# Performance work log

Measured on AMD Instinct MI355X. Metric: run time of the kernel, lower is better.

The kernel has to match this reference:

```python
import jax, jax.numpy as jnp
import numpy as np

H, W, R = 512, 512, 4
H8, W8 = H // 8, W // 8  # 64, 64
B, C = 4, 256


def _offsets(r):
    # diamond window: y in [-r, r], x in [|y|-r, r-|y|]  ->  2r^2+2r+1 offsets
    offs = []
    for y in range(-r, r + 1):
        for x in range(abs(y) - r, r - abs(y) + 1):
            offs.append((y, x))
    return np.asarray(offs, dtype=np.float32)  # [L, 2] = (dy, dx)

_OFFS = _offsets(R)  # L = 41


def _corr_pyramid(f1, f2):
    # over the second image's spatial dims for each pyramid level.
    c = jnp.einsum('bcij,bcuv->bijuv', f1, f2) / jnp.sqrt(jnp.float32(f1.shape[1]))
    pyr = [c]
    for _ in range(3):
        b, i, j, h, w = pyr[-1].shape
        pyr.append(pyr[-1].reshape(b, i, j, h // 2, 2, w // 2, 2).mean(axis=(4, 6)))
    return pyr  # shapes [B,64,64,64/2^k,64/2^k] for k=0..3


def _bilinear_zeros(volf, py, px, h, w):
    # volf: [B,H8,W8,h*w]; py/px: [B,H8,W8,L] pixel coords; zero padding.
    y0 = jnp.floor(py); x0 = jnp.floor(px)
    wy1 = py - y0; wy0 = 1.0 - wy1
    wx1 = px - x0; wx0 = 1.0 - wx1

    def gather(yi, xi):
        valid = (yi >= 0) & (yi < h) & (xi >= 0) & (xi < w)
        yc = jnp.clip(yi, 0, h - 1).astype(jnp.int32)
        xc = jnp.clip(xi, 0, w - 1).astype(jnp.int32)
        v = jnp.take_along_axis(volf, yc * w + xc, axis=-1)
        return jnp.where(valid, v, jnp.zeros((), volf.dtype))

    return (wy0 * wx0 * gather(y0, x0) + wy0 * wx1 * gather(y0, x0 + 1)
            + wy1 * wx0 * gather(y0 + 1, x0) + wy1 * wx1 * gather(y0 + 1, x0 + 1))


def _lookup_level(corr, flow, k):
    # corr: [B,H8,W8,h,w]; flow: [B,2,H8,W8] (chan 0 = dy, chan 1 = dx)
    b, _, _, h, w = corr.shape
    dy = jnp.asarray(_OFFS[:, 0]); dx = jnp.asarray(_OFFS[:, 1])
    ii = jnp.arange(H8, dtype=corr.dtype)[:, None]   # [H8,1]
    jj = jnp.arange(W8, dtype=corr.dtype)[None, :]   # [1,W8]
    scale = jnp.float32(2.0 ** k)
    yc = (ii[None] + flow[:, 0]) / scale             # [B,H8,W8]
    xc = (jj[None] + flow[:, 1]) / scale
    py = yc[..., None] + dy                          # [B,H8,W8,L]
    px = xc[..., None] + dx
    # original normalizes by dim/2 (not (dim-1)/2), grid_sample align_corners=True
    # maps normalized g -> pixel (g+1)*(dim-1)/2, net: pixel = coord*(dim-1)/dim
    py = py * (h - 1) / h
    px = px * (w - 1) / w
    volf = corr.reshape(b, H8, W8, h * w)
    return _bilinear_zeros(volf, py, px, h, w)       # [B,H8,W8,L]


def setup_inputs() -> dict:
    key = jax.random.key(0)
    k1, k2, k3 = jax.random.split(key, 3)
    feat1 = jax.random.normal(k1, (B, C, H8, W8), dtype=jnp.float32)
    feat2 = jax.random.normal(k2, (B, C, H8, W8), dtype=jnp.float32)
    curr_flow = jax.random.normal(k3, (B, 2, H8, W8), dtype=jnp.float32)
    return {"feat1": feat1, "feat2": feat2, "curr_flow": curr_flow}


def reference(feat1, feat2, curr_flow):
    pyr = _corr_pyramid(feat1, feat2)
    lookups = [_lookup_level(pyr[k], curr_flow, k) for k in range(4)]
    return jnp.stack(lookups, axis=3)  # [B, H8, W8, 4, 41]
```

## Files before the change

kernel.cpp:

```cpp
#include <hip/hip_runtime.h>
#include <stdint.h>

#define NB 4
#define NC 256
#define TC 5440

typedef short bf16x8 __attribute__((ext_vector_type(8)));
typedef float f32x4  __attribute__((ext_vector_type(4)));

__device__ __forceinline__ unsigned short f2b(float x){
  uint32_t u = __float_as_uint(x);
  return (unsigned short)((u + 0x7FFFu + ((u >> 16) & 1u)) >> 16);
}

__global__ __launch_bounds__(256) void prep_all(const float* __restrict__ f1,
                 const float* __restrict__ f2,
                 unsigned short* __restrict__ f1t,
                 unsigned short* __restrict__ f2p){
  __shared__ float lds[128*65];
  const int t = threadIdx.x;
  const int bx = blockIdx.x;

  if (bx < 2048){
    const int b = bx >> 9, rest = bx & 511;
    const int cc = rest >> 7, pt = rest & 127;
    const int p0 = pt*32, c0 = cc*64;
    const int tx = t & 31, ty = t >> 5;
    float (*tileF)[33] = (float(*)[33])lds;
    #pragma unroll
    for (int r = 0; r < 8; ++r){
      int c = ty + r*8;
      tileF[c][tx] = f1[((size_t)(b*NC) + c0 + c)*4096 + p0 + tx];
    }
    __syncthreads();
    #pragma unroll
    for (int r = 0; r < 4; ++r){
      int pl = ty + r*8;
      size_t o = ((size_t)(b*4096 + p0 + pl))*NC;
      unsigned int v = (unsigned int)f2b(tileF[2*tx][pl])
                     | ((unsigned int)f2b(tileF[2*tx+1][pl]) << 16);
      *(unsigned int*)(f1t + o + c0 + 2*tx) = v;
    }
  } else {
    const int fid = bx - 2048;
    const int b = fid >> 7, rest = fid & 127;
    const int reg = rest >> 2, cc = rest & 3;
    const int i0 = (reg >> 2) * 8, j0 = (reg & 3) * 16;
    const int c0 = cc * 64;

    #pragma unroll
    for (int it = 0; it < 8; ++it){
      int q = t + 256*it;
      int ch = q >> 5, rc = q & 31, ri = rc >> 2, c4 = rc & 3;
      const float4 v = *(const float4*)(f2 + ((size_t)(b*NC) + c0 + ch)*4096
                                          + (i0+ri)*64 + j0 + c4*4);
      float* dstL = lds + (ri*16 + c4*4)*65 + ch;
      dstL[0] = v.x; dstL[65] = v.y; dstL[130] = v.z; dstL[195] = v.w;
    }
    __syncthreads();
    unsigned short* f2pB = f2p + (size_t)b*TC*NC;

    {
      const int u = t & 31, cb = t >> 5;
      #pragma unroll
      for (int it = 0; it < 16; ++it){
        int l = cb + 8*it;
        int ci = l >> 4, cj = l & 15;
        unsigned int v = (unsigned int)f2b(lds[l*65 + 2*u])
                       | ((unsigned int)f2b(lds[l*65 + 2*u + 1]) << 16);
        *(unsigned int*)(f2pB + ((size_t)((i0+ci)*64 + j0+cj))*NC + c0 + 2*u) = v;
      }
    }
    #pragma unroll
    for (int it = 0; it < 8; ++it){
      int idx = t + 256*it;
      int cl = idx >> 6, ch = idx & 63;
      int a = cl >> 3, bc = cl & 7;
      const float* p00 = lds + ((2*a)*16 + 2*bc)*65 + ch;
      float s = p00[0] + p00[65] + p00[16*65] + p00[17*65];
      f2pB[((size_t)(4096 + ((i0>>1)+a)*32 + (j0>>1)+bc))*NC + c0 + ch] = f2b(s*0.25f);
    }
    #pragma unroll
    for (int it = 0; it < 2; ++it){
      int idx = t + 256*it;
      int cl = idx >> 6, ch = idx & 63;
      int a = cl >> 2, bc = cl & 3;
      float s = 0.f;
      #pragma unroll
      for (int dy2 = 0; dy2 < 4; ++dy2)
        #pragma unroll
        for (int dx2 = 0; dx2 < 4; ++dx2)
          s += lds[((4*a+dy2)*16 + 4*bc+dx2)*65 + ch];
      f2pB[((size_t)(5120 + ((i0>>2)+a)*16 + (j0>>2)+bc))*NC + c0 + ch] = f2b(s*0.0625f);
    }
    if (t < 128){
      int cl = t >> 6, ch = t & 63;
      float s = 0.f;
      #pragma unroll
      for (int dy3 = 0; dy3 < 8; ++dy3)
        #pragma unroll
        for (int dx3 = 0; dx3 < 8; ++dx3)
          s += lds[(dy3*16 + 8*cl + dx3)*65 + ch];
      f2pB[((size_t)(5376 + (i0>>3)*8 + (j0>>3) + cl))*NC + c0 + ch] = f2b(s*(1.0f/64.0f));
    }
  }
}

__global__ __launch_bounds__(256, 4) void lookup_main(const float* __restrict__ flow,
                 const unsigned short* __restrict__ f1t,
                 const unsigned short* __restrict__ f2p,
                 float* __restrict__ out){
  const int lane = threadIdx.x & 63;
  const int wid  = threadIdx.x >> 6;
  const int blk = blockIdx.x;
  const int xs = blk & 7;
  const int bb = xs >> 1;
  const int tile = ((blk >> 3) << 1) | (xs & 1);
  const int ti4 = (tile >> 4) << 2;
  const int tj4 = (tile & 15) << 2;

  __shared__ float box[4*16*112];
  __shared__ int   ls_y0[64], ls_x0[64];
  __shared__ float ls_f[32];
  __shared__ int   ls_meta[32];

  {
    float4* b4 = (float4*)box;
    for (int q = threadIdx.x; q < (4*16*112)/4; q += 256)
      b4[q] = make_float4(0.f, 0.f, 0.f, 0.f);
  }

  const int n = lane & 15;
  const int g = lane >> 4;
  const int pn = ((ti4 + (n >> 2)) << 6) + tj4 + (n & 3);

  bf16x8 bfr[8];
  {
    const unsigned short* f1c = f1t + ((size_t)(bb*4096 + pn))*NC;
    #pragma unroll
    for (int st = 0; st < 8; ++st)
      bfr[st] = *(const bf16x8*)(f1c + st*32 + g*8);
  }

  if (wid == 0){
    const int k = g;
    const int i_n = pn >> 6, j_n = pn & 63;
    const float fy = flow[((bb*2 + 0)*64 + i_n)*64 + j_n];
    const float fx = flow[((bb*2 + 1)*64 + i_n)*64 + j_n];
    if (k == 0){ ls_f[n] = fy; ls_f[16 + n] = fx; }
    const int h = 64 >> k;
    const float inv = 1.0f / (float)(1 << k);
    const float s = (float)(h - 1) / (float)h;
    const float yc = ((float)i_n + fy) * inv;
    const float xc = ((float)j_n + fx) * inv;
    const int y0 = (int)floorf((yc - 4.0f) * s);
    const int x0 = (int)floorf((xc - 4.0f) * s);
    ls_y0[k*16 + n] = y0;
    ls_x0[k*16 + n] = x0;
    int ymin = y0, ymax = y0, xmin = x0, xmax = x0;
    #pragma unroll
    for (int m = 1; m < 16; m <<= 1){
      ymin = min(ymin, __shfl_xor(ymin, m));
      ymax = max(ymax, __shfl_xor(ymax, m));
      xmin = min(xmin, __shfl_xor(xmin, m));
      xmax = max(xmax, __shfl_xor(xmax, m));
    }
    if (n == 0){
      int ylo = max(ymin, 0), yhi = min(ymax + 9, h - 1);
      int xlo = max(xmin, 0), xhi = min(xmax + 9, h - 1);
      int H = max(yhi - ylo + 1, 0), W = max(xhi - xlo + 1, 0);
      int cells = W * H;
      ls_meta[k*8 + 0] = ylo;
      ls_meta[k*8 + 1] = xlo;
      ls_meta[k*8 + 2] = W;
      ls_meta[k*8 + 3] = cells;
      ls_meta[k*8 + 4] = __float_as_int(1.0f / (float)W);
      ls_meta[k*8 + 5] = (k==0) ? 0 : (k==1) ? 4096 : (k==2) ? 5120 : 5376;
      ls_meta[k*8 + 6] = (cells + 15) >> 4;
    }
  }
  __syncthreads();

  const int y0n0 = ls_y0[n],      x0n0 = ls_x0[n];
  const int y0n1 = ls_y0[16 + n], x0n1 = ls_x0[16 + n];
  const int y0n2 = ls_y0[32 + n], x0n2 = ls_x0[32 + n];
  const int y0n3 = ls_y0[48 + n], x0n3 = ls_x0[48 + n];
  const int pre1 = ls_meta[6];
  const int pre2 = pre1 + ls_meta[14];
  const int pre3 = pre2 + ls_meta[22];
  const int P    = pre3 + ls_meta[30];

  for (int p = wid; p < P; p += 4){
    const int k  = (p >= pre1) + (p >= pre2) + (p >= pre3);
    const int lp = p - ((k==0) ? 0 : (k==1) ? pre1 : (k==2) ? pre2 : pre3);
    const int mb = k*8;
    const int ylo = ls_meta[mb], xlo = ls_meta[mb+1], W = ls_meta[mb+2];
    const int cells = ls_meta[mb+3];
    const float rW = __int_as_float(ls_meta[mb+4]);
    const int lvo = ls_meta[mb+5];
    const int h = 64 >> k;
    const int base = lp << 4;

    const int idxA = min(base + n, cells - 1);
    const int by = (int)fmaf((float)idxA, rW, 0.004f);
    const int bx = idxA - by*W;
    const unsigned short* col = f2p + ((size_t)bb*TC + lvo + (ylo + by)*h + (xlo + bx))*NC;

    f32x4 acc0 = {0.f,0.f,0.f,0.f}, acc1 = {0.f,0.f,0.f,0.f};
    #pragma unroll
    for (int st = 0; st < 8; st += 2){
      bf16x8 a0 = *(const bf16x8*)(col + st*32 + g*8);
      bf16x8 a1 = *(const bf16x8*)(col + (st+1)*32 + g*8);
      acc0 = __builtin_amdgcn_mfma_f32_16x16x32_bf16(a0, bfr[st],   acc0, 0, 0, 0);
      acc1 = __builtin_amdgcn_mfma_f32_16x16x32_bf16(a1, bfr[st+1], acc1, 0, 0, 0);
    }
    const int yb = (k==0) ? y0n0 : (k==1) ? y0n1 : (k==2) ? y0n2 : y0n3;
    const int xb = (k==0) ? x0n0 : (k==1) ? x0n1 : (k==2) ? x0n2 : x0n3;
    #pragma unroll
    for (int r = 0; r < 4; ++r){
      const int ci = base + (g << 2) + r;
      if (ci < cells){
        const int byc = (int)fmaf((float)ci, rW, 0.004f);
        const int bxc = ci - byc*W;
        const int ry = ylo + byc - yb;
        const int rx = xlo + bxc - xb;
        if ((unsigned)ry < 10u && (unsigned)rx < 10u)
          box[(k*16 + n)*112 + ry*10 + rx] = (acc0[r] + acc1[r]) * 0.0625f;
      }
    }
  }
  __syncthreads();

  int dy = 0, dx = 0;
  {
    int rem = lane;
    #pragma unroll
    for (int ry = -4; ry <= 4; ++ry){
      int ab = ry < 0 ? -ry : ry;
      int ln = 9 - 2*ab;
      if (rem >= 0 && rem < ln){ dy = ry; dx = rem + (ab - 4); }
      rem -= ln;
    }
  }
  const int k = wid;
  const float inv = 1.0f / (float)(1 << k);
  const float s = (float)((64 >> k) - 1) / (float)(64 >> k);
  if (lane < 41){
    for (int t = 0; t < 16; ++t){
      const int pt = ((ti4 + (t >> 2)) << 6) + tj4 + (t & 3);
      const float fy = ls_f[t], fx = ls_f[16 + t];
      const float yc = ((float)(pt >> 6) + fy) * inv;
      const float xc = ((float)(pt & 63) + fx) * inv;
      const float py = (yc + (float)dy) * s;
      const float px = (xc + (float)dx) * s;
      const float fy0 = floorf(py), fx0 = floorf(px);
      const float wy1 = py - fy0, wx1 = px - fx0;
      const float wy0 = 1.0f - wy1, wx0 = 1.0f - wx1;
      const int iy = (int)fy0 - ls_y0[k*16 + t];
      const int ix = (int)fx0 - ls_x0[k*16 + t];
      const float* bx_ = &box[(k*16 + t)*112 + iy*10 + ix];
      const float v = wy0*(wx0*bx_[0] + wx1*bx_[1]) + wy1*(wx0*bx_[10] + wx1*bx_[11]);
      out[((size_t)(bb*4096 + pt)*4 + k)*41 + lane] = v;
    }
  }
}

extern "C" void kernel_launch(void* const* d_in, const int* in_sizes, int n_in,
                              void* d_out, int out_size, void* d_ws, size_t ws_size,
                              hipStream_t stream){
  const float* feat1 = (const float*)d_in[0];
  const float* feat2 = (const float*)d_in[1];
  const float* flow  = (const float*)d_in[2];
  float* out = (float*)d_out;
  unsigned short* f1t = (unsigned short*)d_ws;
  unsigned short* f2p = f1t + (size_t)NB*4096*NC;

  prep_all<<<2560, 256, 0, stream>>>(feat1, feat2, f1t, f2p);
  lookup_main<<<1024, 256, 0, stream>>>(flow, f1t, f2p, out);
}
```

Measured before the change: 125.6 us.

## Split lookup blocks per pyramid level to shrink LDS and raise parallelism

Each lookup block now handles a single pyramid level for its 16-pixel tile, and the grid grows to four times as many blocks. Every wave computes the per-level bounding box itself with shuffles, so the serial wave-0 metadata phase and its shared-memory table go away. The per-block box buffer shrinks to one level with a 113 stride to cut LDS bank conflicts, and the final interpolation spreads the 16 pixels across the four waves. In exchange, the f1 fragment and flow loads are repeated four times across blocks, and the coarse-level blocks get very little MFMA work.

```diff
diff --git a/kernel.cpp b/kernel.cpp
--- a/kernel.cpp
+++ b/kernel.cpp
@@ -115,18 +115,19 @@
   const int blk = blockIdx.x;
   const int xs = blk & 7;
   const int bb = xs >> 1;
-  const int tile = ((blk >> 3) << 1) | (xs & 1);
+  const int r8 = blk >> 3;
+  const int k  = r8 & 3;
+  const int tile = ((r8 >> 2) << 1) | (xs & 1);
   const int ti4 = (tile >> 4) << 2;
   const int tj4 = (tile & 15) << 2;
 
-  __shared__ float box[4*16*112];
-  __shared__ int   ls_y0[64], ls_x0[64];
+  __shared__ float box[16*113 + 4];
   __shared__ float ls_f[32];
-  __shared__ int   ls_meta[32];
+  __shared__ int   ls_y0[16], ls_x0[16];
 
   {
     float4* b4 = (float4*)box;
-    for (int q = threadIdx.x; q < (4*16*112)/4; q += 256)
+    for (int q = threadIdx.x; q < (16*113 + 4)/4; q += 256)
       b4[q] = make_float4(0.f, 0.f, 0.f, 0.f);
   }
 
@@ -142,69 +143,45 @@
       bfr[st] = *(const bf16x8*)(f1c + st*32 + g*8);
   }
 
-  if (wid == 0){
-    const int k = g;
-    const int i_n = pn >> 6, j_n = pn & 63;
-    const float fy = flow[((bb*2 + 0)*64 + i_n)*64 + j_n];
-    const float fx = flow[((bb*2 + 1)*64 + i_n)*64 + j_n];
-    if (k == 0){ ls_f[n] = fy; ls_f[16 + n] = fx; }
-    const int h = 64 >> k;
-    const float inv = 1.0f / (float)(1 << k);
-    const float s = (float)(h - 1) / (float)h;
-    const float yc = ((float)i_n + fy) * inv;
-    const float xc = ((float)j_n + fx) * inv;
-    const int y0 = (int)floorf((yc - 4.0f) * s);
-    const int x0 = (int)floorf((xc - 4.0f) * s);
-    ls_y0[k*16 + n] = y0;
-    ls_x0[k*16 + n] = x0;
-    int ymin = y0, ymax = y0, xmin = x0, xmax = x0;
-    #pragma unroll
-    for (int m = 1; m < 16; m <<= 1){
-      ymin = min(ymin, __shfl_xor(ymin, m));
-      ymax = max(ymax, __shfl_xor(ymax, m));
-      xmin = min(xmin, __shfl_xor(xmin, m));
-      xmax = max(xmax, __shfl_xor(xmax, m));
-    }
-    if (n == 0){
-      int ylo = max(ymin, 0), yhi = min(ymax + 9, h - 1);
-      int xlo = max(xmin, 0), xhi = min(xmax + 9, h - 1);
-      int H = max(yhi - ylo + 1, 0), W = max(xhi - xlo + 1, 0);
-      int cells = W * H;
-      ls_meta[k*8 + 0] = ylo;
-      ls_meta[k*8 + 1] = xlo;
-      ls_meta[k*8 + 2] = W;
-      ls_meta[k*8 + 3] = cells;
-      ls_meta[k*8 + 4] = __float_as_int(1.0f / (float)W);
-      ls_meta[k*8 + 5] = (k==0) ? 0 : (k==1) ? 4096 : (k==2) ? 5120 : 5376;
-      ls_meta[k*8 + 6] = (cells + 15) >> 4;
-    }
+  const int h = 64 >> k;
+  const float inv = 1.0f / (float)(1 << k);
+  const float s = (float)(h - 1) / (float)h;
+  const int i_n = pn >> 6, j_n = pn & 63;
+  const float fy = flow[((bb*2 + 0)*64 + i_n)*64 + j_n];
+  const float fx = flow[((bb*2 + 1)*64 + i_n)*64 + j_n];
+  const float yc = ((float)i_n + fy) * inv;
+  const float xc = ((float)j_n + fx) * inv;
+  const int y0 = (int)floorf((yc - 4.0f) * s);
+  const int x0 = (int)floorf((xc - 4.0f) * s);
+  int ymin = y0, ymax = y0, xmin = x0, xmax = x0;
+  #pragma unroll
+  for (int m = 1; m < 16; m <<= 1){
+    ymin = min(ymin, __shfl_xor(ymin, m));
+    ymax = max(ymax, __shfl_xor(ymax, m));
+    xmin = min(xmin, __shfl_xor(xmin, m));
+    xmax = max(xmax, __shfl_xor(xmax, m));
+  }
+  const int ylo = max(ymin, 0), yhi = min(ymax + 9, h - 1);
+  const int xlo = max(xmin, 0), xhi = min(xmax + 9, h - 1);
+  const int W = max(xhi - xlo + 1, 0);
+  const int cells = W * max(yhi - ylo + 1, 0);
+  const float rW = 1.0f / (float)W;
+  const int lvo = (k==0) ? 0 : (k==1) ? 4096 : (k==2) ? 5120 : 5376;
+  const unsigned short* lv = f2p + ((size_t)bb*TC + lvo)*NC;
+
+  if (threadIdx.x < 16){
+    ls_f[n] = fy; ls_f[16 + n] = fx;
+    ls_y0[n] = y0; ls_x0[n] = x0;
   }
   __syncthreads();
 
-  const int y0n0 = ls_y0[n],      x0n0 = ls_x0[n];
-  const int y0n1 = ls_y0[16 + n], x0n1 = ls_x0[16 + n];
-  const int y0n2 = ls_y0[32 + n], x0n2 = ls_x0[32 + n];
-  const int y0n3 = ls_y0[48 + n], x0n3 = ls_x0[48 + n];
-  const int pre1 = ls_meta[6];
-  const int pre2 = pre1 + ls_meta[14];
-  const int pre3 = pre2 + ls_meta[22];
-  const int P    = pre3 + ls_meta[30];
-
+  const int P = (cells + 15) >> 4;
   for (int p = wid; p < P; p += 4){
-    const int k  = (p >= pre1) + (p >= pre2) + (p >= pre3);
-    const int lp = p - ((k==0) ? 0 : (k==1) ? pre1 : (k==2) ? pre2 : pre3);
-    const int mb = k*8;
-    const int ylo = ls_meta[mb], xlo = ls_meta[mb+1], W = ls_meta[mb+2];
-    const int cells = ls_meta[mb+3];
-    const float rW = __int_as_float(ls_meta[mb+4]);
-    const int lvo = ls_meta[mb+5];
-    const int h = 64 >> k;
-    const int base = lp << 4;
-
+    const int base = p << 4;
     const int idxA = min(base + n, cells - 1);
     const int by = (int)fmaf((float)idxA, rW, 0.004f);
     const int bx = idxA - by*W;
-    const unsigned short* col = f2p + ((size_t)bb*TC + lvo + (ylo + by)*h + (xlo + bx))*NC;
+    const unsigned short* col = lv + (size_t)((ylo + by)*h + (xlo + bx))*NC;
 
     f32x4 acc0 = {0.f,0.f,0.f,0.f}, acc1 = {0.f,0.f,0.f,0.f};
     #pragma unroll
@@ -214,18 +191,16 @@
       acc0 = __builtin_amdgcn_mfma_f32_16x16x32_bf16(a0, bfr[st],   acc0, 0, 0, 0);
       acc1 = __builtin_amdgcn_mfma_f32_16x16x32_bf16(a1, bfr[st+1], acc1, 0, 0, 0);
     }
-    const int yb = (k==0) ? y0n0 : (k==1) ? y0n1 : (k==2) ? y0n2 : y0n3;
-    const int xb = (k==0) ? x0n0 : (k==1) ? x0n1 : (k==2) ? x0n2 : x0n3;
     #pragma unroll
     for (int r = 0; r < 4; ++r){
       const int ci = base + (g << 2) + r;
       if (ci < cells){
         const int byc = (int)fmaf((float)ci, rW, 0.004f);
         const int bxc = ci - byc*W;
-        const int ry = ylo + byc - yb;
-        const int rx = xlo + bxc - xb;
+        const int ry = ylo + byc - y0;
+        const int rx = xlo + bxc - x0;
         if ((unsigned)ry < 10u && (unsigned)rx < 10u)
-          box[(k*16 + n)*112 + ry*10 + rx] = (acc0[r] + acc1[r]) * 0.0625f;
+          box[n*113 + ry*10 + rx] = (acc0[r] + acc1[r]) * 0.0625f;
       }
     }
   }
@@ -242,23 +217,22 @@
       rem -= ln;
     }
   }
-  const int k = wid;
-  const float inv = 1.0f / (float)(1 << k);
-  const float s = (float)((64 >> k) - 1) / (float)(64 >> k);
   if (lane < 41){
-    for (int t = 0; t < 16; ++t){
+    #pragma unroll
+    for (int tt = 0; tt < 4; ++tt){
+      const int t = wid*4 + tt;
       const int pt = ((ti4 + (t >> 2)) << 6) + tj4 + (t & 3);
-      const float fy = ls_f[t], fx = ls_f[16 + t];
-      const float yc = ((float)(pt >> 6) + fy) * inv;
-      const float xc = ((float)(pt & 63) + fx) * inv;
-      const float py = (yc + (float)dy) * s;
-      const float px = (xc + (float)dx) * s;
+      const float fyt = ls_f[t], fxt = ls_f[16 + t];
+      const float yct = ((float)(pt >> 6) + fyt) * inv;
+      const float xct = ((float)(pt & 63) + fxt) * inv;
+      const float py = (yct + (float)dy) * s;
+      const float px = (xct + (float)dx) * s;
       const float fy0 = floorf(py), fx0 = floorf(px);
       const float wy1 = py - fy0, wx1 = px - fx0;
       const float wy0 = 1.0f - wy1, wx0 = 1.0f - wx1;
-      const int iy = (int)fy0 - ls_y0[k*16 + t];
-      const int ix = (int)fx0 - ls_x0[k*16 + t];
-      const float* bx_ = &box[(k*16 + t)*112 + iy*10 + ix];
+      const int iy = (int)fy0 - ls_y0[t];
+      const int ix = (int)fx0 - ls_x0[t];
+      const float* bx_ = &box[t*113 + iy*10 + ix];
       const float v = wy0*(wx0*bx_[0] + wx1*bx_[1]) + wy1*(wx0*bx_[10] + wx1*bx_[11]);
       out[((size_t)(bb*4096 + pt)*4 + k)*41 + lane] = v;
     }
@@ -276,5 +250,5 @@
   unsigned short* f2p = f1t + (size_t)NB*4096*NC;
 
   prep_all<<<2560, 256, 0, stream>>>(feat1, feat2, f1t, f2p);
-  lookup_main<<<1024, 256, 0, stream>>>(flow, f1t, f2p, out);
-}
+  lookup_main<<<4096, 256, 0, stream>>>(flow, f1t, f2p, out);
+}
```

After: 152.7 us. 1.22x slower.

## Store f2 pyramid in channel-chunk-major layout for coalesced MFMA gathers

Applied to the files above, without the earlier changes.

The pooled f2 pyramid changes from cell-major with 256 contiguous channels to a per-level layout of 8-channel chunks, cell-major within each chunk. Neighbouring cells read by adjacent lanes in the lookup kernel then fall on contiguous 16-byte segments rather than rows 512 bytes apart, which should improve load coalescing in the gather loop. The prep kernel now builds each pyramid level from the level above through small LDS buffers and writes 16-byte vector stores. The per-point LDS box stride is padded from 112 to 113 to reduce bank conflicts. The extra LDS and barriers in prep add some cost there.

```diff
diff --git a/kernel.cpp b/kernel.cpp
--- a/kernel.cpp
+++ b/kernel.cpp
@@ -3,7 +3,10 @@
 
 #define NB 4
 #define NC 256
-#define TC 5440
+#define FB   1392640
+#define LVO1 1048576
+#define LVO2 1310720
+#define LVO3 1376256
 
 typedef short bf16x8 __attribute__((ext_vector_type(8)));
 typedef float f32x4  __attribute__((ext_vector_type(4)));
@@ -12,12 +15,17 @@
   uint32_t u = __float_as_uint(x);
   return (unsigned short)((u + 0x7FFFu + ((u >> 16) & 1u)) >> 16);
 }
+__device__ __forceinline__ unsigned int pack2(float a, float b){
+  return (unsigned int)f2b(a) | ((unsigned int)f2b(b) << 16);
+}
 
 __global__ __launch_bounds__(256) void prep_all(const float* __restrict__ f1,
                  const float* __restrict__ f2,
                  unsigned short* __restrict__ f1t,
-                 unsigned short* __restrict__ f2p){
+                 unsigned short* __restrict__ f2c){
   __shared__ float lds[128*65];
+  __shared__ float l1s[32*65];
+  __shared__ float l2s[8*65];
   const int t = threadIdx.x;
   const int bx = blockIdx.x;
 
@@ -37,16 +45,14 @@
     for (int r = 0; r < 4; ++r){
       int pl = ty + r*8;
       size_t o = ((size_t)(b*4096 + p0 + pl))*NC;
-      unsigned int v = (unsigned int)f2b(tileF[2*tx][pl])
-                     | ((unsigned int)f2b(tileF[2*tx+1][pl]) << 16);
-      *(unsigned int*)(f1t + o + c0 + 2*tx) = v;
+      *(unsigned int*)(f1t + o + c0 + 2*tx) = pack2(tileF[2*tx][pl], tileF[2*tx+1][pl]);
     }
   } else {
     const int fid = bx - 2048;
     const int b = fid >> 7, rest = fid & 127;
     const int reg = rest >> 2, cc = rest & 3;
     const int i0 = (reg >> 2) * 8, j0 = (reg & 3) * 16;
-    const int c0 = cc * 64;
+    const int c0 = cc * 64, qb = cc * 8;
 
     #pragma unroll
     for (int it = 0; it < 8; ++it){
@@ -58,57 +64,77 @@
       dstL[0] = v.x; dstL[65] = v.y; dstL[130] = v.z; dstL[195] = v.w;
     }
     __syncthreads();
-    unsigned short* f2pB = f2p + (size_t)b*TC*NC;
-
+    unsigned short* f2cB = f2c + (size_t)b*FB;
+
+    #pragma unroll
+    for (int it = 0; it < 4; ++it){
+      int idx = t + 256*it;
+      int cell = idx & 127, qi = idx >> 7;
+      int ci = cell >> 4, cj = cell & 15;
+      const float* src = lds + cell*65 + qi*8;
+      uint4 v;
+      v.x = pack2(src[0], src[1]); v.y = pack2(src[2], src[3]);
+      v.z = pack2(src[4], src[5]); v.w = pack2(src[6], src[7]);
+      int cellg = (i0+ci)*64 + j0+cj;
+      *(uint4*)(f2cB + ((size_t)(qb+qi)*4096 + cellg)*8) = v;
+    }
     {
-      const int u = t & 31, cb = t >> 5;
+      int cell = t & 31, qi = t >> 5;
+      int a = cell >> 3, bc = cell & 7;
+      const float* p00 = lds + ((2*a)*16 + 2*bc)*65 + qi*8;
+      float s[8];
       #pragma unroll
-      for (int it = 0; it < 16; ++it){
-        int l = cb + 8*it;
-        int ci = l >> 4, cj = l & 15;
-        unsigned int v = (unsigned int)f2b(lds[l*65 + 2*u])
-                       | ((unsigned int)f2b(lds[l*65 + 2*u + 1]) << 16);
-        *(unsigned int*)(f2pB + ((size_t)((i0+ci)*64 + j0+cj))*NC + c0 + 2*u) = v;
+      for (int j = 0; j < 8; ++j){
+        s[j] = p00[j] + p00[65+j] + p00[16*65+j] + p00[17*65+j];
+        l1s[cell*65 + qi*8 + j] = s[j];
       }
-    }
-    #pragma unroll
-    for (int it = 0; it < 8; ++it){
-      int idx = t + 256*it;
-      int cl = idx >> 6, ch = idx & 63;
-      int a = cl >> 3, bc = cl & 7;
-      const float* p00 = lds + ((2*a)*16 + 2*bc)*65 + ch;
-      float s = p00[0] + p00[65] + p00[16*65] + p00[17*65];
-      f2pB[((size_t)(4096 + ((i0>>1)+a)*32 + (j0>>1)+bc))*NC + c0 + ch] = f2b(s*0.25f);
-    }
-    #pragma unroll
-    for (int it = 0; it < 2; ++it){
-      int idx = t + 256*it;
-      int cl = idx >> 6, ch = idx & 63;
-      int a = cl >> 2, bc = cl & 3;
-      float s = 0.f;
+      uint4 v;
+      v.x = pack2(s[0]*0.25f, s[1]*0.25f); v.y = pack2(s[2]*0.25f, s[3]*0.25f);
+      v.z = pack2(s[4]*0.25f, s[5]*0.25f); v.w = pack2(s[6]*0.25f, s[7]*0.25f);
+      int cellg = ((i0>>1)+a)*32 + (j0>>1)+bc;
+      *(uint4*)(f2cB + LVO1 + ((size_t)(qb+qi)*1024 + cellg)*8) = v;
+    }
+    __syncthreads();
+    if (t < 64){
+      int cell = t & 7, qi = t >> 3;
+      int a2 = cell >> 2, bc2 = cell & 3;
+      float s[8];
       #pragma unroll
-      for (int dy2 = 0; dy2 < 4; ++dy2)
-        #pragma unroll
-        for (int dx2 = 0; dx2 < 4; ++dx2)
-          s += lds[((4*a+dy2)*16 + 4*bc+dx2)*65 + ch];
-      f2pB[((size_t)(5120 + ((i0>>2)+a)*16 + (j0>>2)+bc))*NC + c0 + ch] = f2b(s*0.0625f);
-    }
-    if (t < 128){
-      int cl = t >> 6, ch = t & 63;
-      float s = 0.f;
+      for (int j = 0; j < 8; ++j){
+        int ch = qi*8 + j;
+        s[j] = l1s[((2*a2)*8   + 2*bc2  )*65 + ch] + l1s[((2*a2)*8   + 2*bc2+1)*65 + ch]
+             + l1s[((2*a2+1)*8 + 2*bc2  )*65 + ch] + l1s[((2*a2+1)*8 + 2*bc2+1)*65 + ch];
+        l2s[cell*65 + ch] = s[j];
+      }
+      uint4 v;
+      v.x = pack2(s[0]*0.0625f, s[1]*0.0625f); v.y = pack2(s[2]*0.0625f, s[3]*0.0625f);
+      v.z = pack2(s[4]*0.0625f, s[5]*0.0625f); v.w = pack2(s[6]*0.0625f, s[7]*0.0625f);
+      int cellg = ((i0>>2)+a2)*16 + (j0>>2)+bc2;
+      *(uint4*)(f2cB + LVO2 + ((size_t)(qb+qi)*256 + cellg)*8) = v;
+    }
+    __syncthreads();
+    if (t < 16){
+      int cl = t & 1, qi = t >> 1;
+      float s[8];
       #pragma unroll
-      for (int dy3 = 0; dy3 < 8; ++dy3)
-        #pragma unroll
-        for (int dx3 = 0; dx3 < 8; ++dx3)
-          s += lds[(dy3*16 + 8*cl + dx3)*65 + ch];
-      f2pB[((size_t)(5376 + (i0>>3)*8 + (j0>>3) + cl))*NC + c0 + ch] = f2b(s*(1.0f/64.0f));
+      for (int j = 0; j < 8; ++j){
+        int ch = qi*8 + j;
+        s[j] = l2s[(0*4 + 2*cl)*65 + ch] + l2s[(0*4 + 2*cl+1)*65 + ch]
+             + l2s[(1*4 + 2*cl)*65 + ch] + l2s[(1*4 + 2*cl+1)*65 + ch];
+      }
+      const float m = 1.0f/64.0f;
+      uint4 v;
+      v.x = pack2(s[0]*m, s[1]*m); v.y = pack2(s[2]*m, s[3]*m);
+      v.z = pack2(s[4]*m, s[5]*m); v.w = pack2(s[6]*m, s[7]*m);
+      int cellg = (i0>>3)*8 + (j0>>3) + cl;
+      *(uint4*)(f2cB + LVO3 + ((size_t)(qb+qi)*64 + cellg)*8) = v;
     }
   }
 }
 
 __global__ __launch_bounds__(256, 4) void lookup_main(const float* __restrict__ flow,
                  const unsigned short* __restrict__ f1t,
-                 const unsigned short* __restrict__ f2p,
+                 const unsigned short* __restrict__ f2c,
                  float* __restrict__ out){
   const int lane = threadIdx.x & 63;
   const int wid  = threadIdx.x >> 6;
@@ -119,14 +145,14 @@
   const int ti4 = (tile >> 4) << 2;
   const int tj4 = (tile & 15) << 2;
 
-  __shared__ float box[4*16*112];
+  __shared__ float box[4*16*113];
   __shared__ int   ls_y0[64], ls_x0[64];
   __shared__ float ls_f[32];
   __shared__ int   ls_meta[32];
 
   {
     float4* b4 = (float4*)box;
-    for (int q = threadIdx.x; q < (4*16*112)/4; q += 256)
+    for (int q = threadIdx.x; q < (4*16*113)/4; q += 256)
       b4[q] = make_float4(0.f, 0.f, 0.f, 0.f);
   }
 
@@ -175,7 +201,7 @@
       ls_meta[k*8 + 2] = W;
       ls_meta[k*8 + 3] = cells;
       ls_meta[k*8 + 4] = __float_as_int(1.0f / (float)W);
-      ls_meta[k*8 + 5] = (k==0) ? 0 : (k==1) ? 4096 : (k==2) ? 5120 : 5376;
+      ls_meta[k*8 + 5] = (k==0) ? 0 : (k==1) ? LVO1 : (k==2) ? LVO2 : LVO3;
       ls_meta[k*8 + 6] = (cells + 15) >> 4;
     }
   }
@@ -189,6 +215,7 @@
   const int pre2 = pre1 + ls_meta[14];
   const int pre3 = pre2 + ls_meta[22];
   const int P    = pre3 + ls_meta[30];
+  const unsigned short* f2cB = f2c + (size_t)bb*FB;
 
   for (int p = wid; p < P; p += 4){
     const int k  = (p >= pre1) + (p >= pre2) + (p >= pre3);
@@ -197,20 +224,23 @@
     const int ylo = ls_meta[mb], xlo = ls_meta[mb+1], W = ls_meta[mb+2];
     const int cells = ls_meta[mb+3];
     const float rW = __int_as_float(ls_meta[mb+4]);
-    const int lvo = ls_meta[mb+5];
+    const int lvoc = ls_meta[mb+5];
     const int h = 64 >> k;
+    const int ncl = h*h;
     const int base = lp << 4;
 
     const int idxA = min(base + n, cells - 1);
     const int by = (int)fmaf((float)idxA, rW, 0.004f);
     const int bx = idxA - by*W;
-    const unsigned short* col = f2p + ((size_t)bb*TC + lvo + (ylo + by)*h + (xlo + bx))*NC;
+    const int cellIdx = (ylo + by)*h + (xlo + bx);
+    const unsigned short* colp = f2cB + lvoc + ((size_t)(g*ncl + cellIdx) << 3);
+    const int strideS = ncl << 5;
 
     f32x4 acc0 = {0.f,0.f,0.f,0.f}, acc1 = {0.f,0.f,0.f,0.f};
     #pragma unroll
     for (int st = 0; st < 8; st += 2){
-      bf16x8 a0 = *(const bf16x8*)(col + st*32 + g*8);
-      bf16x8 a1 = *(const bf16x8*)(col + (st+1)*32 + g*8);
+      bf16x8 a0 = *(const bf16x8*)(colp + (size_t)st*strideS);
+      bf16x8 a1 = *(const bf16x8*)(colp + (size_t)(st+1)*strideS);
       acc0 = __builtin_amdgcn_mfma_f32_16x16x32_bf16(a0, bfr[st],   acc0, 0, 0, 0);
       acc1 = __builtin_amdgcn_mfma_f32_16x16x32_bf16(a1, bfr[st+1], acc1, 0, 0, 0);
     }
@@ -225,7 +255,7 @@
         const int ry = ylo + byc - yb;
         const int rx = xlo + bxc - xb;
         if ((unsigned)ry < 10u && (unsigned)rx < 10u)
-          box[(k*16 + n)*112 + ry*10 + rx] = (acc0[r] + acc1[r]) * 0.0625f;
+          box[(k*16 + n)*113 + ry*10 + rx] = (acc0[r] + acc1[r]) * 0.0625f;
       }
     }
   }
@@ -258,7 +288,7 @@
       const float wy0 = 1.0f - wy1, wx0 = 1.0f - wx1;
       const int iy = (int)fy0 - ls_y0[k*16 + t];
       const int ix = (int)fx0 - ls_x0[k*16 + t];
-      const float* bx_ = &box[(k*16 + t)*112 + iy*10 + ix];
+      const float* bx_ = &box[(k*16 + t)*113 + iy*10 + ix];
       const float v = wy0*(wx0*bx_[0] + wx1*bx_[1]) + wy1*(wx0*bx_[10] + wx1*bx_[11]);
       out[((size_t)(bb*4096 + pt)*4 + k)*41 + lane] = v;
     }
@@ -273,8 +303,8 @@
   const float* flow  = (const float*)d_in[2];
   float* out = (float*)d_out;
   unsigned short* f1t = (unsigned short*)d_ws;
-  unsigned short* f2p = f1t + (size_t)NB*4096*NC;
-
-  prep_all<<<2560, 256, 0, stream>>>(feat1, feat2, f1t, f2p);
-  lookup_main<<<1024, 256, 0, stream>>>(flow, f1t, f2p, out);
-}
+  unsigned short* f2c = f1t + (size_t)NB*4096*NC;
+
+  prep_all<<<2560, 256, 0, stream>>>(feat1, feat2, f1t, f2c);
+  lookup_main<<<1024, 256, 0, stream>>>(flow, f1t, f2c, out);
+}
```

Measured after the change: 111.2 us. 11.5% less time.
